# Kernel optimization log

Measured on AMD Instinct MI355X. Metric: run time of the kernel, lower is better.

The kernel has to match this reference:

```python
import jax, jax.numpy as jnp
import numpy as np

GAMMAS = (0.01, 0.1, 1.0, 10.0, 100.0)
FOCAL_GAMMA = 2.0
SMOOTH = 0.1
TASK_W = (0.4, 0.3, 0.3)
A_RECON, A_ORTH, A_ADV = 1.0, 0.1, 0.1
NUM_DOMAINS = 4
NUM_LABELS1 = 4


def focal_smooth(logits, targets, maskf):
    # FocalLoss.forward with smoothing > 0, masked mean
    n_classes = logits.shape[1]
    log_p = jax.nn.log_softmax(logits, axis=1)
    p = jnp.exp(log_p)
    onehot = jax.nn.one_hot(targets, n_classes, dtype=logits.dtype)
    smooth = onehot * (1.0 - SMOOTH) + SMOOTH / n_classes
    ce = -(smooth * log_p).sum(axis=1)
    pt = jnp.take_along_axis(p, targets[:, None], axis=1)[:, 0]
    loss = ce * (1.0 - pt) ** FOCAL_GAMMA
    return (loss * maskf).sum() / jnp.maximum(maskf.sum(), 1.0)


def ce_masked(logits, targets, maskf):
    log_p = jax.nn.log_softmax(logits, axis=1)
    nll = -jnp.take_along_axis(log_p, targets[:, None], axis=1)[:, 0]
    return (nll * maskf).sum() / jnp.maximum(maskf.sum(), 1.0)


def cond_mmd(feats, domains, labels, maskf):
    # Global pairwise sq-distance matrix; multi-gamma RBF kernels summed.
    sq = (feats ** 2).sum(axis=-1)                      # (B,)
    Dmat = sq[:, None] + sq[None, :] - 2.0 * feats @ feats.T  # (B,B)
    Ksum = jnp.zeros_like(Dmat)
    for g in GAMMAS:
        Ksum = Ksum + jnp.exp(-g * Dmat)
    loss = jnp.asarray(0.0, feats.dtype)
    count = jnp.asarray(0.0, feats.dtype)
    for lab in range(NUM_LABELS1):
        lm = (labels == lab).astype(feats.dtype) * maskf
        for d1 in range(NUM_DOMAINS):
            m1 = lm * (domains == d1).astype(feats.dtype)
            n1 = m1.sum()
            Km1 = Ksum @ m1
            for d2 in range(d1 + 1, NUM_DOMAINS):
                m2 = lm * (domains == d2).astype(feats.dtype)
                n2 = m2.sum()
                valid = (n1 > 1) & (n2 > 1)
                term = (m1 @ Km1) / jnp.maximum(n1, 1.0) ** 2 \
                     + (m2 @ (Ksum @ m2)) / jnp.maximum(n2, 1.0) ** 2 \
                     - 2.0 * (m2 @ Km1) / jnp.maximum(n1 * n2, 1.0)
                loss = loss + jnp.where(valid, term, 0.0)
                count = count + valid.astype(feats.dtype)
    return loss / jnp.maximum(count, 1.0)


def hsic(c, s):
    n = c.shape[0]
    c = c / jnp.maximum(jnp.linalg.norm(c, axis=-1, keepdims=True), 1e-12)
    s = s / jnp.maximum(jnp.linalg.norm(s, axis=-1, keepdims=True), 1e-12)
    K = c @ c.T
    L = s @ s.T
    Kc = K - K.mean(axis=0, keepdims=True) - K.mean(axis=1, keepdims=True) + K.mean()
    Lc = L - L.mean(axis=0, keepdims=True) - L.mean(axis=1, keepdims=True) + L.mean()
    return (Kc * Lc).sum() / (n - 1) ** 2


def setup_inputs() -> dict:
    key = jax.random.key(0)
    ks = jax.random.split(key, 20)
    B, D, H = 4096, 256, 768
    inp = {
        'logits1': jax.random.normal(ks[0], (B, 4), jnp.float32),
        'labels1': jax.random.randint(ks[1], (B,), 0, 4),
        'logits2': jax.random.normal(ks[2], (B, 6), jnp.float32),
        'labels2': jax.random.randint(ks[3], (B,), 0, 6),
        'logits3': jax.random.normal(ks[4], (B, 3), jnp.float32),
        'labels3': jax.random.randint(ks[5], (B,), 0, 3),
        'c_v': jax.random.normal(ks[6], (B, D), jnp.float32),
        's_v': jax.random.normal(ks[7], (B, D), jnp.float32),
        'c_t': jax.random.normal(ks[8], (B, D), jnp.float32),
        's_t': jax.random.normal(ks[9], (B, D), jnp.float32),
        'v_sv': jax.random.normal(ks[10], (B, NUM_DOMAINS), jnp.float32),
        'v_st': jax.random.normal(ks[11], (B, NUM_DOMAINS), jnp.float32),
        'domain_labels': jax.random.randint(ks[12], (B,), 0, NUM_DOMAINS),
        'mask': jnp.ones((B,), dtype=bool),
        'h_img_recon': jax.random.normal(ks[13], (B, H), jnp.float32),
        'h_img_orig': jax.random.normal(ks[14], (B, H), jnp.float32),
        'h_txt_recon': jax.random.normal(ks[15], (B, H), jnp.float32),
        'h_txt_orig': jax.random.normal(ks[16], (B, H), jnp.float32),
    }
    return inp


def reference(logits1, labels1, logits2, labels2, logits3, labels3,
              c_v, s_v, c_t, s_t, v_sv, v_st, domain_labels, mask,
              h_img_recon, h_img_orig, h_txt_recon, h_txt_orig):
    maskf = mask.astype(jnp.float32)
    total = jnp.asarray(0.0, jnp.float32)
    # classification (focal + label smoothing), per-task weighted
    total = total + TASK_W[0] * focal_smooth(logits1, labels1, maskf)
    total = total + TASK_W[1] * focal_smooth(logits2, labels2, maskf)
    total = total + TASK_W[2] * focal_smooth(logits3, labels3, maskf)
    # adversarial: CE on spurious domain logits + conditional MMD on causal feats
    l_adv_s = ce_masked(v_sv, domain_labels, maskf) + ce_masked(v_st, domain_labels, maskf)
    l_adv_c = cond_mmd(c_v, domain_labels, labels1, maskf) \
            + cond_mmd(c_t, domain_labels, labels1, maskf)
    total = total + A_ADV * (l_adv_s + l_adv_c)
    # orthogonality (HSIC), on unmasked features as in source
    l_orth = hsic(c_v, s_v) + hsic(c_t, s_t)
    total = total + A_ORTH * l_orth
    # reconstruction MSE
    l_recon = jnp.mean((h_img_recon - h_img_orig) ** 2) + jnp.mean((h_txt_recon - h_txt_orig) ** 2)
    total = total + A_RECON * l_recon
    return total
```

## Files before the change

kernel.cpp:

```cpp
#include <hip/hip_runtime.h>
#include <hip/hip_bf16.h>


typedef short bf16x8 __attribute__((ext_vector_type(8)));
typedef float f32x4 __attribute__((ext_vector_type(4)));
typedef unsigned long long u64;
typedef unsigned int u32;

static constexpr int D = 256;
static constexpr int H = 768;
static constexpr int NG = 16;
static constexpr float FX32 = 4294967296.f;
static constexpr float IFX32 = 2.3283064365386963e-10f;

__device__ inline void gAddFx(u64* p, float v) {
  long long q = (long long)llroundf(v * FX32);
  atomicAdd(p, (u64)q);
}
__device__ inline float fxToF(u64 v) { return (float)(long long)v * IFX32; }

__device__ inline float focal_n(const float* x, int n, int tgt,
                                float s_over_n, float oms) {
  float mx = x[0];
  for (int c = 1; c < n; ++c) mx = fmaxf(mx, x[c]);
  float se = 0.f, sx = 0.f;
  for (int c = 0; c < n; ++c) { se += __expf(x[c] - mx); sx += x[c]; }
  float logZ = mx + __logf(se);
  float ce = logZ - oms * x[tgt] - s_over_n * sx;
  float pt = __expf(x[tgt] - logZ);
  float om = 1.f - pt;
  return ce * om * om;
}

extern "C" __global__ __launch_bounds__(256) void k_pre(
    const void* __restrict__ mask, const int* __restrict__ y1,
    const int* __restrict__ dom,
    const float* __restrict__ l1, const float* __restrict__ l2,
    const float* __restrict__ l3, const int* __restrict__ y2,
    const int* __restrict__ y3,
    const float* __restrict__ vsv, const float* __restrict__ vst,
    const float* __restrict__ cv, const float* __restrict__ sv,
    const float* __restrict__ ct, const float* __restrict__ st,
    const float* __restrict__ ir, const float* __restrict__ io,
    const float* __restrict__ trc, const float* __restrict__ to,
    u64* SA, u64* GCU, u64* U64,
    int* gid, float* sq, float* inv, unsigned short* bf,
    int B, int N4, int NA, int NB) {
  __shared__ u32 sh3[3];
  __shared__ u32 cnt[NG];
  __shared__ int redi[4];
  __shared__ float redf[4];
  int bid = blockIdx.x;
  int t = threadIdx.x;

  if (bid < NA) {
    if (t < 3) sh3[t] = 0;
    if (t < NG) cnt[t] = 0;
    __syncthreads();
    u32 a = 0, b2 = 0, cd = 0;
    if (t * 16 + 15 < B) {
      uint4 wv = ((const uint4*)mask)[t];
      u32 ws[4] = {wv.x, wv.y, wv.z, wv.w};
      #pragma unroll
      for (int j = 0; j < 4; ++j) {
        a |= ws[j] & 0xffu; b2 |= ws[j] & 0xff00u; cd |= ws[j] & 0xffff0000u;
      }
    }
    if (a) atomicOr(&sh3[0], 1u);
    if (b2) atomicOr(&sh3[1], 1u);
    if (cd) atomicOr(&sh3[2], 1u);
    __syncthreads();
    int mode;
    if ((sh3[1] | sh3[2]) == 0) mode = 0;
    else if (sh3[0] == 0 && sh3[1] == 0) mode = 1;
    else mode = 2;
    int r = bid * 256 + t;
    int mi = 0;
    float s[5] = {0.f, 0.f, 0.f, 0.f, 0.f};
    if (r < B) {
      if (mode == 0)      mi = ((const int*)mask)[r] ? 1 : 0;
      else if (mode == 1) mi = (((const float*)mask)[r] != 0.f) ? 1 : 0;
      else                mi = ((const unsigned char*)mask)[r] ? 1 : 0;
      int g = -1;
      if (mi) { g = y1[r] * 4 + dom[r]; atomicAdd(&cnt[g], 1u); }
      gid[r] = g;
      if (mi) {
        float x[6];
        for (int c = 0; c < 4; ++c) x[c] = l1[r * 4 + c];
        s[0] = focal_n(x, 4, y1[r], 0.1f / 4.f, 0.9f);
        for (int c = 0; c < 6; ++c) x[c] = l2[r * 6 + c];
        s[1] = focal_n(x, 6, y2[r], 0.1f / 6.f, 0.9f);
        for (int c = 0; c < 3; ++c) x[c] = l3[r * 3 + c];
        s[2] = focal_n(x, 3, y3[r], 0.1f / 3.f, 0.9f);
        int d = dom[r];
        for (int c = 0; c < 4; ++c) x[c] = vsv[r * 4 + c];
        {
          float mx = fmaxf(fmaxf(x[0], x[1]), fmaxf(x[2], x[3]));
          float se = __expf(x[0]-mx)+__expf(x[1]-mx)+__expf(x[2]-mx)+__expf(x[3]-mx);
          s[3] = mx + __logf(se) - x[d];
        }
        for (int c = 0; c < 4; ++c) x[c] = vst[r * 4 + c];
        {
          float mx = fmaxf(fmaxf(x[0], x[1]), fmaxf(x[2], x[3]));
          float se = __expf(x[0]-mx)+__expf(x[1]-mx)+__expf(x[2]-mx)+__expf(x[3]-mx);
          s[4] = mx + __logf(se) - x[d];
        }
      }
    }
    int v = mi;
    #pragma unroll
    for (int o = 32; o > 0; o >>= 1) v += __shfl_down(v, o);
    if ((t & 63) == 0) redi[t >> 6] = v;
    __syncthreads();
    if (t == 0) atomicAdd(&SA[5], (u64)(redi[0] + redi[1] + redi[2] + redi[3]));
    if (t < NG && cnt[t]) atomicAdd(&GCU[t], (u64)cnt[t]);
    for (int k = 0; k < 5; ++k) {
      float x = s[k];
      #pragma unroll
      for (int o = 32; o > 0; o >>= 1) x += __shfl_down(x, o);
      __syncthreads();
      if ((t & 63) == 0) redf[t >> 6] = x;
      __syncthreads();
      if (t == 0) gAddFx(&SA[k], redf[0] + redf[1] + redf[2] + redf[3]);
    }
  } else if (bid < NA + NB) {
    int b = bid - NA;
    int f = b >> 6;
    int rb = b & 63;
    const float* p = (f == 0) ? cv : (f == 1) ? sv : (f == 2) ? ct : st;
    int w = t >> 6, L = t & 63;
    float up0 = 0.f, up1 = 0.f, up2 = 0.f, up3 = 0.f;
    for (int k = 0; k < 16; ++k) {
      int r = rb * 64 + w * 16 + k;
      float4 v = ((const float4*)(p + (size_t)r * D))[L];
      float ss = v.x * v.x + v.y * v.y + v.z * v.z + v.w * v.w;
      #pragma unroll
      for (int o = 32; o > 0; o >>= 1) ss += __shfl_down(ss, o);
      ss = __shfl(ss, 0);
      float iv = 1.f / fmaxf(sqrtf(ss), 1e-12f);
      if ((f & 1) == 0) {
        int fi = f >> 1;
        alignas(8) __hip_bfloat16 hb[4];
        hb[0] = __float2bfloat16(v.x); hb[1] = __float2bfloat16(v.y);
        hb[2] = __float2bfloat16(v.z); hb[3] = __float2bfloat16(v.w);
        *(uint2*)(bf + ((size_t)fi * B + r) * D + L * 4) = *(uint2*)hb;
        if (L == 0) sq[fi * B + r] = ss;
      }
      if (L == 0) inv[f * B + r] = iv;
      up0 += v.x * iv; up1 += v.y * iv; up2 += v.z * iv; up3 += v.w * iv;
    }
    u64* Uf = U64 + f * D + 4 * L;
    gAddFx(Uf + 0, up0); gAddFx(Uf + 1, up1);
    gAddFx(Uf + 2, up2); gAddFx(Uf + 3, up3);
  } else {
    int cidx = bid - (NA + NB);
    int j = cidx >> 8;
    int cb = cidx & 255;
    const float4* A  = (const float4*)(j ? trc : ir);
    const float4* Bp = (const float4*)(j ? to : io);
    float acc = 0.f;
    for (int idx = cb * 256 + t; idx < N4; idx += 256 * 256) {
      float4 a = A[idx], b = Bp[idx];
      float dx = a.x-b.x, dy = a.y-b.y, dz = a.z-b.z, dw = a.w-b.w;
      acc += dx*dx + dy*dy + dz*dz + dw*dw;
    }
    #pragma unroll
    for (int o = 32; o > 0; o >>= 1) acc += __shfl_down(acc, o);
    if ((t & 63) == 0) redf[t >> 6] = acc;
    __syncthreads();
    if (t == 0) gAddFx(&SA[6 + j], redf[0] + redf[1] + redf[2] + redf[3]);
  }
}

extern "C" __global__ __launch_bounds__(256) void k_big(
    const float* __restrict__ cv, const float* __restrict__ sv,
    const float* __restrict__ ct, const float* __restrict__ st,
    const float* __restrict__ inv, u64* M64,
    const unsigned short* __restrict__ bf, const float* __restrict__ sq,
    const int* __restrict__ gid, u64* GSP, int B) {
  __shared__ __align__(16) char smem[38016];
  int bid = blockIdx.x;
  int tid = threadIdx.x;

  if (bid < 512) {
    float (*lc)[16] = (float(*)[16])smem;
    float* lis = (float*)(smem + 16384);
    int p = bid >> 8;
    int a0 = ((bid >> 4) & 15) * 16;
    int i0 = (bid & 15) * 256;
    const float* c = p ? ct : cv;
    const float* s = p ? st : sv;
    const float* ic = inv + (2 * p) * B;
    const float* is = inv + (2 * p + 1) * B;
    int t = tid;
    if (t < 256) lis[t] = is[i0 + t];
    for (int e = t; e < 256 * 16; e += 256) {
      int i = e >> 4, rr = e & 15;
      lc[i][rr] = c[(size_t)(i0 + i) * D + a0 + rr] * ic[i0 + i];
    }
    __syncthreads();
    float4 acc[4];
    #pragma unroll
    for (int r = 0; r < 4; ++r) acc[r] = make_float4(0.f, 0.f, 0.f, 0.f);
    #pragma unroll 8
    for (int i = 0; i < 256; ++i) {
      float svv = s[(size_t)(i0 + i) * D + t] * lis[i];
      const float4* lr = (const float4*)lc[i];
      #pragma unroll
      for (int r = 0; r < 4; ++r) {
        float4 c4 = lr[r];
        acc[r].x += c4.x * svv; acc[r].y += c4.y * svv;
        acc[r].z += c4.z * svv; acc[r].w += c4.w * svv;
      }
    }
    u64* Mp = M64 + (size_t)p * D * D;
    #pragma unroll
    for (int r = 0; r < 4; ++r) {
      gAddFx(&Mp[(a0 + 4 * r + 0) * D + t], acc[r].x);
      gAddFx(&Mp[(a0 + 4 * r + 1) * D + t], acc[r].y);
      gAddFx(&Mp[(a0 + 4 * r + 2) * D + t], acc[r].z);
      gAddFx(&Mp[(a0 + 4 * r + 3) * D + t], acc[r].w);
    }
    return;
  }

  unsigned short* Ab = (unsigned short*)smem;
  unsigned short* Bb = (unsigned short*)(smem + 16384);
  u32 (*gsw)[264] = (u32(*)[264])(smem + 32768);
  int*   gA = (int*)(smem + 36992);
  int*   gB = gA + 64;
  float* sA = (float*)(gB + 64);
  float* sB = sA + 64;

  int idx2 = bid - 512;
  int feat = idx2 & 1;
  int tlin = idx2 >> 1;
  int NT = B / 64;
  float tf = (float)tlin;
  int ti = (int)((2.f * NT + 1.f -
                  sqrtf((2.f * NT + 1.f) * (2.f * NT + 1.f) - 8.f * tf)) * 0.5f);
  while (ti > 0 && (ti * NT - (ti * (ti - 1)) / 2) > tlin) --ti;
  while (((ti + 1) * NT - ((ti + 1) * ti) / 2) <= tlin) ++ti;
  int tj = ti + (tlin - (ti * NT - (ti * (ti - 1)) / 2));
  int i0 = ti * 64, j0 = tj * 64;
  bool diag = (ti == tj);
  const unsigned short* fb = bf + (size_t)feat * B * D;
  const float* sqf = sq + (size_t)feat * B;

  int w = tid >> 6, L = tid & 63, m = L & 15, q = L >> 4;

  {
    u32* gz = (u32*)gsw;
    for (int e = tid; e < 4 * 264; e += 256) gz[e] = 0;
    if (tid < 64) { gA[tid] = gid[i0 + tid]; sA[tid] = sqf[i0 + tid]; }
    else if (tid < 128) { int r = tid - 64; gB[r] = gid[j0 + r]; sB[r] = sqf[j0 + r]; }
  }

  f32x4 acc[4] = {{0.f,0.f,0.f,0.f},{0.f,0.f,0.f,0.f},{0.f,0.f,0.f,0.f},{0.f,0.f,0.f,0.f}};

  for (int h = 0; h < 2; ++h) {
    if (h) __syncthreads();
    for (int e = tid; e < 1024; e += 256) {
      int row = e >> 4, ck = e & 15;
      uint4 v = *(const uint4*)(fb + (size_t)(i0 + row) * D + h * 128 + ck * 8);
      *(uint4*)&Ab[row * 128 + ((ck ^ (row & 15)) * 8)] = v;
    }
    if (!diag) {
      for (int e = tid; e < 1024; e += 256) {
        int row = e >> 4, ck = e & 15;
        uint4 v = *(const uint4*)(fb + (size_t)(j0 + row) * D + h * 128 + ck * 8);
        *(uint4*)&Bb[row * 128 + ((ck ^ (row & 15)) * 8)] = v;
      }
    }
    __syncthreads();
    const unsigned short* Bp = diag ? Ab : Bb;
    #pragma unroll
    for (int kk = 0; kk < 4; ++kk) {
      int ar = w * 16 + m;
      bf16x8 aF = *(const bf16x8*)&Ab[ar * 128 + (((kk * 4 + q) ^ (ar & 15)) * 8)];
      #pragma unroll
      for (int c = 0; c < 4; ++c) {
        int br = c * 16 + m;
        bf16x8 bF = *(const bf16x8*)&Bp[br * 128 + (((kk * 4 + q) ^ (br & 15)) * 8)];
        acc[c] = __builtin_amdgcn_mfma_f32_16x16x32_bf16(aF, bF, acc[c], 0, 0, 0);
      }
    }
  }
  int ri0 = w * 16 + q * 4;
  int gi0 = gA[ri0], gi1 = gA[ri0+1], gi2 = gA[ri0+2], gi3 = gA[ri0+3];
  float si0 = sA[ri0], si1 = sA[ri0+1], si2 = sA[ri0+2], si3 = sA[ri0+3];
  int giv[4] = {gi0, gi1, gi2, gi3};
  float siv[4] = {si0, si1, si2, si3};
  #pragma unroll
  for (int c = 0; c < 4; ++c) {
    int rj = c * 16 + m;
    int gj = gB[rj];
    float sb = sB[rj];
    #pragma unroll
    for (int v = 0; v < 4; ++v) {
      int ri = ri0 + v;
      int gi = giv[v];
      if (gi >= 0 && gj >= 0 && !(diag && ri > rj)) {
        float K;
        if (diag && ri == rj) K = 5.f;
        else {
          float d = fmaxf(siv[v] + sb - 2.f * acc[c][v], 0.f);
          K = __expf(-0.01f * d) + __expf(-0.1f * d) + __expf(-d)
            + __expf(-10.f * d) + __expf(-100.f * d);
        }
        u32 kf = (u32)(K * 65536.f + 0.5f);
        int a = min(gi, gj), b = max(gi, gj);
        atomicAdd(&gsw[w][a * NG + b], kf);
      }
    }
  }
  __syncthreads();
  if (tid < NG * NG) {
    u64 s = (u64)gsw[0][tid] + gsw[1][tid] + gsw[2][tid] + gsw[3][tid];
    if (s)
      atomicAdd(&GSP[((size_t)(tlin & 63) * 2 + feat) * NG * NG + tid], s);
  }
}

extern "C" __global__ __launch_bounds__(256) void k_hsic(
    const u64* __restrict__ U64, const u64* __restrict__ M64, u64* SA) {
  __shared__ float red[8];
  __shared__ float ush[32], vsh[D];
  int p = blockIdx.y;
  int k0 = blockIdx.x * 32;
  int t = threadIdx.x;
  vsh[t] = fxToF(U64[(2 * p + 1) * D + t]);
  if (t < 32) ush[t] = fxToF(U64[(2 * p) * D + k0 + t]);
  __syncthreads();
  const u64* Mp = M64 + (size_t)p * D * D;
  float trkl = 0.f, cr = 0.f;
  #pragma unroll 4
  for (int k = 0; k < 32; ++k) {
    float mv = fxToF(Mp[(size_t)(k0 + k) * D + t]);
    trkl += mv * mv;
    cr += ush[k] * mv;
  }
  cr *= vsh[t];
  #pragma unroll
  for (int o = 32; o > 0; o >>= 1) { trkl += __shfl_down(trkl, o); cr += __shfl_down(cr, o); }
  if ((t & 63) == 0) { red[t >> 6] = trkl; red[4 + (t >> 6)] = cr; }
  __syncthreads();
  if (t == 0) gAddFx(&SA[10 + p], red[0] + red[1] + red[2] + red[3]);
  if (t == 64) gAddFx(&SA[12 + p], red[4] + red[5] + red[6] + red[7]);
}

extern "C" __global__ __launch_bounds__(256) void k_final(
    const u64* SA, const u64* GCU, const u64* GSP,
    const u64* U64, float* out, int B) {
  __shared__ float red[8];
  __shared__ float gssh[2 * NG * NG];
  int t = threadIdx.x;
  for (int e = t; e < 2 * NG * NG; e += 256) {
    u64 ssum = 0;
    int f = e >> 8, idx = e & 255;
    for (int cpy = 0; cpy < 64; ++cpy)
      ssum += GSP[((size_t)cpy * 2 + f) * NG * NG + idx];
    gssh[e] = (float)((double)ssum * (1.0 / 65536.0));
  }
  __syncthreads();

  float n = (float)B;
  float hs[2];
  for (int p = 0; p < 2; ++p) {
    float ut = fxToF(U64[(2 * p) * D + t]);
    float vt = fxToF(U64[(2 * p + 1) * D + t]);
    float uu = ut * ut, vv = vt * vt;
    #pragma unroll
    for (int o = 32; o > 0; o >>= 1) { uu += __shfl_down(uu, o); vv += __shfl_down(vv, o); }
    __syncthreads();
    if ((t & 63) == 0) { red[t >> 6] = uu; red[4 + (t >> 6)] = vv; }
    __syncthreads();
    float uus = red[0] + red[1] + red[2] + red[3];
    float vvs = red[4] + red[5] + red[6] + red[7];
    float trkl = (float)((double)(long long)SA[10 + p] * (double)IFX32);
    float cr   = (float)((double)(long long)SA[12 + p] * (double)IFX32);
    hs[p] = (trkl - (2.f / n) * cr + uus * vvs / (n * n))
          / ((n - 1.f) * (n - 1.f));
    __syncthreads();
  }
  if (t == 0) {
    float msum = fmaxf((float)SA[5], 1.f);
    float f1 = fxToF(SA[0]) / msum;
    float f2 = fxToF(SA[1]) / msum;
    float f3 = fxToF(SA[2]) / msum;
    float cesv = fxToF(SA[3]) / msum;
    float cest = fxToF(SA[4]) / msum;
    float mmd[2];
    for (int f = 0; f < 2; ++f) {
      float loss = 0.f, cntv = 0.f;
      for (int lab = 0; lab < 4; ++lab)
        for (int d1 = 0; d1 < 4; ++d1)
          for (int d2 = d1 + 1; d2 < 4; ++d2) {
            int a = lab * 4 + d1, b = lab * 4 + d2;
            float n1 = (float)GCU[a], n2 = (float)GCU[b];
            if (n1 > 1.f && n2 > 1.f) {
              float g11 = 2.f * gssh[f * 256 + a * NG + a] - 5.f * n1;
              float g22 = 2.f * gssh[f * 256 + b * NG + b] - 5.f * n2;
              float g12 = gssh[f * 256 + a * NG + b];
              loss += g11 / (fmaxf(n1, 1.f) * fmaxf(n1, 1.f))
                    + g22 / (fmaxf(n2, 1.f) * fmaxf(n2, 1.f))
                    - 2.f * g12 / fmaxf(n1 * n2, 1.f);
              cntv += 1.f;
            }
          }
      mmd[f] = loss / fmaxf(cntv, 1.f);
    }
    double rs = ((double)(long long)SA[6] + (double)(long long)SA[7])
              * (double)IFX32;
    float recon = (float)(rs / ((double)B * (double)H));
    float total = 0.4f * f1 + 0.3f * f2 + 0.3f * f3
                + 0.1f * (cesv + cest + mmd[0] + mmd[1])
                + 0.1f * (hs[0] + hs[1])
                + recon;
    out[0] = total;
  }
}

extern "C" void kernel_launch(void* const* d_in, const int* in_sizes, int n_in,
                              void* d_out, int out_size, void* d_ws, size_t ws_size,
                              hipStream_t stream) {
  const float* l1  = (const float*)d_in[0];
  const int*   y1  = (const int*)d_in[1];
  const float* l2  = (const float*)d_in[2];
  const int*   y2  = (const int*)d_in[3];
  const float* l3  = (const float*)d_in[4];
  const int*   y3  = (const int*)d_in[5];
  const float* cv  = (const float*)d_in[6];
  const float* sv  = (const float*)d_in[7];
  const float* ct  = (const float*)d_in[8];
  const float* st  = (const float*)d_in[9];
  const float* vsv = (const float*)d_in[10];
  const float* vst = (const float*)d_in[11];
  const int*   dom = (const int*)d_in[12];
  const void*  mask= d_in[13];
  const float* ir  = (const float*)d_in[14];
  const float* io  = (const float*)d_in[15];
  const float* trc = (const float*)d_in[16];
  const float* to  = (const float*)d_in[17];
  int B = in_sizes[1];

  u64* SA  = (u64*)d_ws;
  u64* GCU = SA + 32;
  u64* U64 = GCU + 16;
  u64* M64 = U64 + 4 * D;
  u64* GSP = M64 + 2 * D * D;
  u64* zend = GSP + 64 * 2 * NG * NG;
  size_t zeroBytes = (size_t)((char*)zend - (char*)d_ws);
  int*   gid = (int*)zend;
  float* sq  = (float*)(gid + B);
  float* inv = sq + 2 * B;
  unsigned short* bf = (unsigned short*)(inv + 4 * B);

  int NA = B / 256;
  int NB = 4 * (B / 64);
  int NC = 512;
  int N4 = B * H / 4;

  hipMemsetAsync(d_ws, 0, zeroBytes, stream);
  k_pre<<<NA + NB + NC, 256, 0, stream>>>(
      mask, y1, dom, l1, l2, l3, y2, y3, vsv, vst,
      cv, sv, ct, st, ir, io, trc, to,
      SA, GCU, U64, gid, sq, inv, bf, B, N4, NA, NB);
  int NT = B / 64;
  int nmmd = 2 * (NT * (NT + 1) / 2);
  k_big<<<512 + nmmd, 256, 0, stream>>>(cv, sv, ct, st, inv, M64,
                                        bf, sq, gid, GSP, B);
  k_hsic<<<dim3(8, 2), 256, 0, stream>>>(U64, M64, SA);
  k_final<<<1, 256, 0, stream>>>(SA, GCU, GSP, U64, (float*)d_out, B);
}
```

Baseline: 253.3 us.

## Sort rows by group before pairwise MMD and accumulate dominant group pairs in registers

Result: slower. 265.5 us (+4.8%).

```diff
diff --git a/kernel.cpp b/kernel.cpp
--- a/kernel.cpp
+++ b/kernel.cpp
@@ -32,9 +32,71 @@
   return ce * om * om;
 }
 
-extern "C" __global__ __launch_bounds__(256) void k_pre(
+extern "C" __global__ __launch_bounds__(1024) void k_prep0(
     const void* __restrict__ mask, const int* __restrict__ y1,
     const int* __restrict__ dom,
+    u64* SA, u64* GCU, int* gid, int* rank, int* gidp,
+    u64* zbase, int zcount, int B) {
+  int t = threadIdx.x;
+  int bid = blockIdx.x;
+  if (bid > 0) {
+    for (int i = (bid - 1) * 1024 + t; i < zcount; i += 32 * 1024)
+      zbase[i] = 0ull;
+    return;
+  }
+  __shared__ u32 sh3[3];
+  __shared__ u32 cnt[17];
+  __shared__ u32 off[17];
+  if (t < 3) sh3[t] = 0;
+  if (t < 17) cnt[t] = 0;
+  if (t < 32) SA[t] = 0ull;
+  __syncthreads();
+  {
+    u32 a = 0, b = 0, cd = 0;
+    const unsigned char* m8 = (const unsigned char*)mask;
+    for (int i = t; i < B; i += 1024) {
+      u32 v = m8[i];
+      int mm = i & 3;
+      if (mm == 0) a |= v; else if (mm == 1) b |= v; else cd |= v;
+    }
+    if (a) atomicOr(&sh3[0], 1u);
+    if (b) atomicOr(&sh3[1], 1u);
+    if (cd) atomicOr(&sh3[2], 1u);
+  }
+  __syncthreads();
+  int mode;
+  if ((sh3[1] | sh3[2]) == 0) mode = 0;
+  else if (sh3[0] == 0 && sh3[1] == 0) mode = 1;
+  else mode = 2;
+  for (int r = t; r < B; r += 1024) {
+    int mi;
+    if (mode == 0)      mi = ((const int*)mask)[r] ? 1 : 0;
+    else if (mode == 1) mi = (((const float*)mask)[r] != 0.f) ? 1 : 0;
+    else                mi = ((const unsigned char*)mask)[r] ? 1 : 0;
+    int g = mi ? (y1[r] * 4 + dom[r]) : -1;
+    gid[r] = g;
+    atomicAdd(&cnt[g < 0 ? 16 : g], 1u);
+  }
+  __syncthreads();
+  if (t == 0) {
+    u32 s = 0;
+    for (int g = 0; g < 16; ++g) { off[g] = s; s += cnt[g]; }
+    off[16] = s;
+    SA[5] = (u64)s;
+  }
+  __syncthreads();
+  if (t < 16) GCU[t] = (u64)cnt[t];
+  for (int r = t; r < B; r += 1024) {
+    int g = gid[r];
+    int slot = g < 0 ? 16 : g;
+    int pos = (int)atomicAdd(&off[slot], 1u);
+    rank[r] = pos;
+    gidp[pos] = g;
+  }
+}
+
+extern "C" __global__ __launch_bounds__(256) void k_pre(
+    const int* __restrict__ y1, const int* __restrict__ dom,
     const float* __restrict__ l1, const float* __restrict__ l2,
     const float* __restrict__ l3, const int* __restrict__ y2,
     const int* __restrict__ y3,
@@ -43,77 +105,39 @@
     const float* __restrict__ ct, const float* __restrict__ st,
     const float* __restrict__ ir, const float* __restrict__ io,
     const float* __restrict__ trc, const float* __restrict__ to,
-    u64* SA, u64* GCU, u64* U64,
-    int* gid, float* sq, float* inv, unsigned short* bf,
+    u64* SA, u64* U64,
+    const int* __restrict__ gid, const int* __restrict__ rank,
+    float* sqp, float* inv, unsigned short* bfp,
     int B, int N4, int NA, int NB) {
-  __shared__ u32 sh3[3];
-  __shared__ u32 cnt[NG];
-  __shared__ int redi[4];
   __shared__ float redf[4];
   int bid = blockIdx.x;
   int t = threadIdx.x;
 
   if (bid < NA) {
-    if (t < 3) sh3[t] = 0;
-    if (t < NG) cnt[t] = 0;
-    __syncthreads();
-    u32 a = 0, b2 = 0, cd = 0;
-    if (t * 16 + 15 < B) {
-      uint4 wv = ((const uint4*)mask)[t];
-      u32 ws[4] = {wv.x, wv.y, wv.z, wv.w};
-      #pragma unroll
-      for (int j = 0; j < 4; ++j) {
-        a |= ws[j] & 0xffu; b2 |= ws[j] & 0xff00u; cd |= ws[j] & 0xffff0000u;
-      }
-    }
-    if (a) atomicOr(&sh3[0], 1u);
-    if (b2) atomicOr(&sh3[1], 1u);
-    if (cd) atomicOr(&sh3[2], 1u);
-    __syncthreads();
-    int mode;
-    if ((sh3[1] | sh3[2]) == 0) mode = 0;
-    else if (sh3[0] == 0 && sh3[1] == 0) mode = 1;
-    else mode = 2;
     int r = bid * 256 + t;
-    int mi = 0;
     float s[5] = {0.f, 0.f, 0.f, 0.f, 0.f};
-    if (r < B) {
-      if (mode == 0)      mi = ((const int*)mask)[r] ? 1 : 0;
-      else if (mode == 1) mi = (((const float*)mask)[r] != 0.f) ? 1 : 0;
-      else                mi = ((const unsigned char*)mask)[r] ? 1 : 0;
-      int g = -1;
-      if (mi) { g = y1[r] * 4 + dom[r]; atomicAdd(&cnt[g], 1u); }
-      gid[r] = g;
-      if (mi) {
-        float x[6];
-        for (int c = 0; c < 4; ++c) x[c] = l1[r * 4 + c];
-        s[0] = focal_n(x, 4, y1[r], 0.1f / 4.f, 0.9f);
-        for (int c = 0; c < 6; ++c) x[c] = l2[r * 6 + c];
-        s[1] = focal_n(x, 6, y2[r], 0.1f / 6.f, 0.9f);
-        for (int c = 0; c < 3; ++c) x[c] = l3[r * 3 + c];
-        s[2] = focal_n(x, 3, y3[r], 0.1f / 3.f, 0.9f);
-        int d = dom[r];
-        for (int c = 0; c < 4; ++c) x[c] = vsv[r * 4 + c];
-        {
-          float mx = fmaxf(fmaxf(x[0], x[1]), fmaxf(x[2], x[3]));
-          float se = __expf(x[0]-mx)+__expf(x[1]-mx)+__expf(x[2]-mx)+__expf(x[3]-mx);
-          s[3] = mx + __logf(se) - x[d];
-        }
-        for (int c = 0; c < 4; ++c) x[c] = vst[r * 4 + c];
-        {
-          float mx = fmaxf(fmaxf(x[0], x[1]), fmaxf(x[2], x[3]));
-          float se = __expf(x[0]-mx)+__expf(x[1]-mx)+__expf(x[2]-mx)+__expf(x[3]-mx);
-          s[4] = mx + __logf(se) - x[d];
-        }
-      }
-    }
-    int v = mi;
-    #pragma unroll
-    for (int o = 32; o > 0; o >>= 1) v += __shfl_down(v, o);
-    if ((t & 63) == 0) redi[t >> 6] = v;
-    __syncthreads();
-    if (t == 0) atomicAdd(&SA[5], (u64)(redi[0] + redi[1] + redi[2] + redi[3]));
-    if (t < NG && cnt[t]) atomicAdd(&GCU[t], (u64)cnt[t]);
+    if (r < B && gid[r] >= 0) {
+      float x[6];
+      for (int c = 0; c < 4; ++c) x[c] = l1[r * 4 + c];
+      s[0] = focal_n(x, 4, y1[r], 0.1f / 4.f, 0.9f);
+      for (int c = 0; c < 6; ++c) x[c] = l2[r * 6 + c];
+      s[1] = focal_n(x, 6, y2[r], 0.1f / 6.f, 0.9f);
+      for (int c = 0; c < 3; ++c) x[c] = l3[r * 3 + c];
+      s[2] = focal_n(x, 3, y3[r], 0.1f / 3.f, 0.9f);
+      int d = dom[r];
+      for (int c = 0; c < 4; ++c) x[c] = vsv[r * 4 + c];
+      {
+        float mx = fmaxf(fmaxf(x[0], x[1]), fmaxf(x[2], x[3]));
+        float se = __expf(x[0]-mx)+__expf(x[1]-mx)+__expf(x[2]-mx)+__expf(x[3]-mx);
+        s[3] = mx + __logf(se) - x[d];
+      }
+      for (int c = 0; c < 4; ++c) x[c] = vst[r * 4 + c];
+      {
+        float mx = fmaxf(fmaxf(x[0], x[1]), fmaxf(x[2], x[3]));
+        float se = __expf(x[0]-mx)+__expf(x[1]-mx)+__expf(x[2]-mx)+__expf(x[3]-mx);
+        s[4] = mx + __logf(se) - x[d];
+      }
+    }
     for (int k = 0; k < 5; ++k) {
       float x = s[k];
       #pragma unroll
@@ -140,11 +164,12 @@
       float iv = 1.f / fmaxf(sqrtf(ss), 1e-12f);
       if ((f & 1) == 0) {
         int fi = f >> 1;
+        int pos = rank[r];
         alignas(8) __hip_bfloat16 hb[4];
         hb[0] = __float2bfloat16(v.x); hb[1] = __float2bfloat16(v.y);
         hb[2] = __float2bfloat16(v.z); hb[3] = __float2bfloat16(v.w);
-        *(uint2*)(bf + ((size_t)fi * B + r) * D + L * 4) = *(uint2*)hb;
-        if (L == 0) sq[fi * B + r] = ss;
+        *(uint2*)(bfp + ((size_t)fi * B + pos) * D + L * 4) = *(uint2*)hb;
+        if (L == 0) sqp[fi * B + pos] = ss;
       }
       if (L == 0) inv[f * B + r] = iv;
       up0 += v.x * iv; up1 += v.y * iv; up2 += v.z * iv; up3 += v.w * iv;
@@ -176,8 +201,8 @@
     const float* __restrict__ cv, const float* __restrict__ sv,
     const float* __restrict__ ct, const float* __restrict__ st,
     const float* __restrict__ inv, u64* M64,
-    const unsigned short* __restrict__ bf, const float* __restrict__ sq,
-    const int* __restrict__ gid, u64* GSP, int B) {
+    const unsigned short* __restrict__ bfp, const float* __restrict__ sqp,
+    const int* __restrict__ gidp, u64* GSP, int B) {
   __shared__ __align__(16) char smem[38016];
   int bid = blockIdx.x;
   int tid = threadIdx.x;
@@ -193,7 +218,7 @@
     const float* ic = inv + (2 * p) * B;
     const float* is = inv + (2 * p + 1) * B;
     int t = tid;
-    if (t < 256) lis[t] = is[i0 + t];
+    lis[t] = is[i0 + t];
     for (int e = t; e < 256 * 16; e += 256) {
       int i = e >> 4, rr = e & 15;
       lc[i][rr] = c[(size_t)(i0 + i) * D + a0 + rr] * ic[i0 + i];
@@ -226,8 +251,8 @@
 
   unsigned short* Ab = (unsigned short*)smem;
   unsigned short* Bb = (unsigned short*)(smem + 16384);
-  u32 (*gsw)[264] = (u32(*)[264])(smem + 32768);
-  int*   gA = (int*)(smem + 36992);
+  u32 (*gsw)[NG * NG] = (u32(*)[NG * NG])(smem + 32768);
+  int*   gA = (int*)(smem + 36864);
   int*   gB = gA + 64;
   float* sA = (float*)(gB + 64);
   float* sB = sA + 64;
@@ -244,16 +269,17 @@
   int tj = ti + (tlin - (ti * NT - (ti * (ti - 1)) / 2));
   int i0 = ti * 64, j0 = tj * 64;
   bool diag = (ti == tj);
-  const unsigned short* fb = bf + (size_t)feat * B * D;
-  const float* sqf = sq + (size_t)feat * B;
+  const unsigned short* fb = bfp + (size_t)feat * B * D;
+  const float* sqf = sqp + (size_t)feat * B;
 
   int w = tid >> 6, L = tid & 63, m = L & 15, q = L >> 4;
 
   {
     u32* gz = (u32*)gsw;
-    for (int e = tid; e < 4 * 264; e += 256) gz[e] = 0;
-    if (tid < 64) { gA[tid] = gid[i0 + tid]; sA[tid] = sqf[i0 + tid]; }
-    else if (tid < 128) { int r = tid - 64; gB[r] = gid[j0 + r]; sB[r] = sqf[j0 + r]; }
+    #pragma unroll
+    for (int e = 0; e < 4; ++e) gz[tid + 256 * e] = 0;
+    if (tid < 64) { gA[tid] = gidp[i0 + tid]; sA[tid] = sqf[i0 + tid]; }
+    else if (tid < 128) { int r = tid - 64; gB[r] = gidp[j0 + r]; sB[r] = sqf[j0 + r]; }
   }
 
   f32x4 acc[4] = {{0.f,0.f,0.f,0.f},{0.f,0.f,0.f,0.f},{0.f,0.f,0.f,0.f},{0.f,0.f,0.f,0.f}};
@@ -286,11 +312,11 @@
       }
     }
   }
+  int ga0 = gA[0], ga1 = gA[63], gb0 = gB[0], gb1 = gB[63];
   int ri0 = w * 16 + q * 4;
-  int gi0 = gA[ri0], gi1 = gA[ri0+1], gi2 = gA[ri0+2], gi3 = gA[ri0+3];
-  float si0 = sA[ri0], si1 = sA[ri0+1], si2 = sA[ri0+2], si3 = sA[ri0+3];
-  int giv[4] = {gi0, gi1, gi2, gi3};
-  float siv[4] = {si0, si1, si2, si3};
+  int giv[4] = {gA[ri0], gA[ri0 + 1], gA[ri0 + 2], gA[ri0 + 3]};
+  float siv[4] = {sA[ri0], sA[ri0 + 1], sA[ri0 + 2], sA[ri0 + 3]};
+  float a00 = 0.f, a01 = 0.f, a10 = 0.f, a11 = 0.f;
   #pragma unroll
   for (int c = 0; c < 4; ++c) {
     int rj = c * 16 + m;
@@ -300,25 +326,49 @@
     for (int v = 0; v < 4; ++v) {
       int ri = ri0 + v;
       int gi = giv[v];
-      if (gi >= 0 && gj >= 0 && !(diag && ri > rj)) {
-        float K;
-        if (diag && ri == rj) K = 5.f;
-        else {
-          float d = fmaxf(siv[v] + sb - 2.f * acc[c][v], 0.f);
-          K = __expf(-0.01f * d) + __expf(-0.1f * d) + __expf(-d)
-            + __expf(-10.f * d) + __expf(-100.f * d);
+      bool on = (gi >= 0) && (gj >= 0) && (!diag || (ri < rj));
+      if (on) {
+        float d = fmaxf(siv[v] + sb - 2.f * acc[c][v], 0.f);
+        float K = __expf(-0.01f * d);
+        if (d < 200.f)
+          K += __expf(-0.1f * d) + __expf(-d) + __expf(-10.f * d)
+             + __expf(-100.f * d);
+        int si_ = (gi == ga0) ? 0 : ((gi == ga1) ? 2 : -4);
+        int sj_ = (gj == gb0) ? 0 : ((gj == gb1) ? 1 : -4);
+        if (si_ >= 0 && sj_ >= 0) {
+          int sel = si_ + sj_;
+          a00 += (sel == 0) ? K : 0.f;
+          a01 += (sel == 1) ? K : 0.f;
+          a10 += (sel == 2) ? K : 0.f;
+          a11 += (sel == 3) ? K : 0.f;
+        } else {
+          atomicAdd(&gsw[w][gi * NG + gj], (u32)(K * 65536.f + 0.5f));
         }
-        u32 kf = (u32)(K * 65536.f + 0.5f);
-        int a = min(gi, gj), b = max(gi, gj);
-        atomicAdd(&gsw[w][a * NG + b], kf);
+      }
+    }
+  }
+  #pragma unroll
+  for (int o = 32; o > 0; o >>= 1) {
+    a00 += __shfl_down(a00, o); a01 += __shfl_down(a01, o);
+    a10 += __shfl_down(a10, o); a11 += __shfl_down(a11, o);
+  }
+  u64* gbase = GSP + ((size_t)(tlin & 63) * 2 + feat) * NG * NG;
+  if (L == 0) {
+    float vals[4] = {a00, a01, a10, a11};
+    int gx[4] = {ga0, ga0, ga1, ga1};
+    int gy[4] = {gb0, gb1, gb0, gb1};
+    #pragma unroll
+    for (int k = 0; k < 4; ++k) {
+      if (vals[k] != 0.f) {
+        int x = min(gx[k], gy[k]), y = max(gx[k], gy[k]);
+        atomicAdd(&gbase[x * NG + y], (u64)(vals[k] * 65536.f + 0.5f));
       }
     }
   }
   __syncthreads();
   if (tid < NG * NG) {
     u64 s = (u64)gsw[0][tid] + gsw[1][tid] + gsw[2][tid] + gsw[3][tid];
-    if (s)
-      atomicAdd(&GSP[((size_t)(tlin & 63) * 2 + feat) * NG * NG + tid], s);
+    if (s) atomicAdd(&gbase[tid], s);
   }
 }
 
@@ -399,8 +449,8 @@
             int a = lab * 4 + d1, b = lab * 4 + d2;
             float n1 = (float)GCU[a], n2 = (float)GCU[b];
             if (n1 > 1.f && n2 > 1.f) {
-              float g11 = 2.f * gssh[f * 256 + a * NG + a] - 5.f * n1;
-              float g22 = 2.f * gssh[f * 256 + b * NG + b] - 5.f * n2;
+              float g11 = 2.f * gssh[f * 256 + a * NG + a] + 5.f * n1;
+              float g22 = 2.f * gssh[f * 256 + b * NG + b] + 5.f * n2;
               float g12 = gssh[f * 256 + a * NG + b];
               loss += g11 / (fmaxf(n1, 1.f) * fmaxf(n1, 1.f))
                     + g22 / (fmaxf(n2, 1.f) * fmaxf(n2, 1.f))
@@ -450,26 +500,29 @@
   u64* M64 = U64 + 4 * D;
   u64* GSP = M64 + 2 * D * D;
   u64* zend = GSP + 64 * 2 * NG * NG;
-  size_t zeroBytes = (size_t)((char*)zend - (char*)d_ws);
-  int*   gid = (int*)zend;
-  float* sq  = (float*)(gid + B);
-  float* inv = sq + 2 * B;
-  unsigned short* bf = (unsigned short*)(inv + 4 * B);
+  int zcount = (int)(zend - U64);
+  int*   gid  = (int*)zend;
+  int*   rank = gid + B;
+  int*   gidp = rank + B;
+  float* sqp  = (float*)(gidp + B);
+  float* inv  = sqp + 2 * B;
+  unsigned short* bfp = (unsigned short*)(inv + 4 * B);
 
   int NA = B / 256;
   int NB = 4 * (B / 64);
   int NC = 512;
   int N4 = B * H / 4;
 
-  hipMemsetAsync(d_ws, 0, zeroBytes, stream);
+  k_prep0<<<33, 1024, 0, stream>>>(mask, y1, dom, SA, GCU, gid, rank, gidp,
+                                   U64, zcount, B);
   k_pre<<<NA + NB + NC, 256, 0, stream>>>(
-      mask, y1, dom, l1, l2, l3, y2, y3, vsv, vst,
+      y1, dom, l1, l2, l3, y2, y3, vsv, vst,
       cv, sv, ct, st, ir, io, trc, to,
-      SA, GCU, U64, gid, sq, inv, bf, B, N4, NA, NB);
+      SA, U64, gid, rank, sqp, inv, bfp, B, N4, NA, NB);
   int NT = B / 64;
   int nmmd = 2 * (NT * (NT + 1) / 2);
   k_big<<<512 + nmmd, 256, 0, stream>>>(cv, sv, ct, st, inv, M64,
-                                        bf, sq, gid, GSP, B);
+                                        bfp, sqp, gidp, GSP, B);
   k_hsic<<<dim3(8, 2), 256, 0, stream>>>(U64, M64, SA);
   k_final<<<1, 256, 0, stream>>>(SA, GCU, GSP, U64, (float*)d_out, B);
 }
```
